# Performance work log

Measured on AMD Instinct MI355X. Metric: run time of the kernel, lower is better.

Reference implementation:

```python
import jax, jax.numpy as jnp
import numpy as np

N_NODES = 50000
N_EDGES = 800000
IN_DIM = 128
HID = 64
OUT = 32
HEADS = 2
NEG_SLOPE = 0.2  # PyG GATConv default


def _gat_layer(x, edge_index, W, a_src, a_dst, b, concat):
    """PyG-style GATConv (add_self_loops=True, eval mode so dropout is a no-op).
    x: [N, F_in], W: [F_in, H*C], a_src/a_dst: [H, C], b: [H*C] or [C].
    """
    N = x.shape[0]
    H, C = a_src.shape
    loops = jnp.arange(N, dtype=edge_index.dtype)
    src = jnp.concatenate([edge_index[0], loops])  # [E+N]
    dst = jnp.concatenate([edge_index[1], loops])

    h = (x @ W).reshape(N, H, C)                   # [N, H, C]
    alpha_src = jnp.sum(h * a_src, axis=-1)        # [N, H]
    alpha_dst = jnp.sum(h * a_dst, axis=-1)        # [N, H]

    e = jax.nn.leaky_relu(alpha_src[src] + alpha_dst[dst], NEG_SLOPE)  # [E+N, H]
    # segment softmax over incoming edges per destination node
    e_max = jax.ops.segment_max(e, dst, num_segments=N)               # [N, H]
    e_exp = jnp.exp(e - e_max[dst])
    denom = jax.ops.segment_sum(e_exp, dst, num_segments=N)           # [N, H]
    alpha = e_exp / denom[dst]                                        # [E+N, H]

    msg = h[src] * alpha[..., None]                                   # [E+N, H, C]
    out = jax.ops.segment_sum(msg, dst, num_segments=N)               # [N, H, C]
    if concat:
        return out.reshape(N, H * C) + b
    return out.mean(axis=1) + b


def setup_inputs() -> dict:
    key = jax.random.key(0)
    ks = jax.random.split(key, 10)
    x = jax.random.normal(ks[0], (N_NODES, IN_DIM), dtype=jnp.float32)
    edge_index = jax.random.randint(ks[1], (2, N_EDGES), 0, N_NODES, dtype=jnp.int64)
    s1 = 1.0 / np.sqrt(IN_DIM)
    s2 = 1.0 / np.sqrt(HEADS * HID)
    return {
        "x": x,
        "edge_index": edge_index,
        "W1": jax.random.normal(ks[2], (IN_DIM, HEADS * HID), dtype=jnp.float32) * s1,
        "a_src1": jax.random.normal(ks[3], (HEADS, HID), dtype=jnp.float32) * s2,
        "a_dst1": jax.random.normal(ks[4], (HEADS, HID), dtype=jnp.float32) * s2,
        "b1": jnp.zeros((HEADS * HID,), dtype=jnp.float32),
        "W2": jax.random.normal(ks[5], (HEADS * HID, OUT), dtype=jnp.float32) * s2,
        "a_src2": jax.random.normal(ks[6], (1, OUT), dtype=jnp.float32) * (1.0 / np.sqrt(OUT)),
        "a_dst2": jax.random.normal(ks[7], (1, OUT), dtype=jnp.float32) * (1.0 / np.sqrt(OUT)),
        "b2": jnp.zeros((OUT,), dtype=jnp.float32),
    }


def reference(x, edge_index, W1, a_src1, a_dst1, b1, W2, a_src2, a_dst2, b2):
    h = _gat_layer(x, edge_index, W1, a_src1, a_dst1, b1, concat=True)   # [N, HEADS*HID]
    h = jax.nn.relu(h)  # dropout is identity in eval mode
    out = _gat_layer(h, edge_index, W2, a_src2, a_dst2, b2, concat=False)  # [N, OUT]
    return out
```

## Files before the change

### kernel.cpp

```cpp
#include <hip/hip_runtime.h>

#define NEG 0.2f

constexpr int NB  = 196;
constexpr int PB  = 4608;
constexpr int EPB = 4096;

using short8 = __attribute__((ext_vector_type(8))) short;
using f32x4  = __attribute__((ext_vector_type(4))) float;

__device__ __forceinline__ ushort f2bf(float f) {
  uint u = __float_as_uint(f);
  return (ushort)((u + 0x7fffu + ((u >> 16) & 1u)) >> 16);
}
__device__ __forceinline__ float bflo(uint u) { return __uint_as_float(u << 16); }
__device__ __forceinline__ float bfhi(uint u) { return __uint_as_float(u & 0xffff0000u); }

__global__ void zero_kernel(int* __restrict__ p, int n)
{
  const int i = threadIdx.x;
  if (i < n) p[i] = 0;
}

__global__ void wt_kernel(const float* __restrict__ W, ushort* __restrict__ wtg)
{
  const int idx = blockIdx.x * 256 + threadIdx.x;
  const int n = idx >> 7, k = idx & 127;
  wtg[idx] = f2bf(W[k * 128 + n]);
}

__global__ __launch_bounds__(256) void binA_kernel(const int* __restrict__ ei,
                                                   int* __restrict__ bcursor,
                                                   int2* __restrict__ tmp, int E)
{
  __shared__ int cnt[NB];
  __shared__ int base[NB];
  const int t = threadIdx.x;
  const int e0 = blockIdx.x * EPB;
  const int e1 = min(e0 + EPB, E);

  if (t < NB) cnt[t] = 0;
  __syncthreads();
  for (int i = e0 + t; i < e1; i += 256)
    atomicAdd(&cnt[ei[E + i] >> 8], 1);
  __syncthreads();
  if (t < NB) {
    const int c = cnt[t];
    if (c > 0) base[t] = atomicAdd(&bcursor[t], c);
    cnt[t] = 0;
  }
  __syncthreads();
  for (int i = e0 + t; i < e1; i += 256) {
    const int s = ei[i];
    const int d = ei[E + i];
    const int b = d >> 8;
    const int pos = base[b] + atomicAdd(&cnt[b], 1);
    tmp[(size_t)b * PB + pos] = make_int2(s, d);
  }
}

__global__ __launch_bounds__(256) void binB_kernel(const int2* __restrict__ tmp,
                                                   const int* __restrict__ bcursor,
                                                   int2* __restrict__ offs2,
                                                   int* __restrict__ ssrc, int N)
{
  __shared__ int cnt[256];
  __shared__ int cur[256];
  __shared__ int sc[256];
  const int b = blockIdx.x;
  const int t = threadIdx.x;
  const int d0 = b << 8;
  const int beg = b * PB;
  const int cE = bcursor[b];

  cnt[t] = 0;
  __syncthreads();
  for (int i = t; i < cE; i += 256)
    atomicAdd(&cnt[tmp[beg + i].y - d0], 1);
  __syncthreads();
  sc[t] = cnt[t];
  __syncthreads();
  for (int off = 1; off < 256; off <<= 1) {
    int v = (t >= off) ? sc[t - off] : 0;
    __syncthreads();
    sc[t] += v;
    __syncthreads();
  }
  const int ebase = sc[t] - cnt[t];
  cur[t] = ebase;
  const int dst = d0 + t;
  if (dst < N) offs2[dst] = make_int2(beg + ebase, beg + ebase + cnt[t]);
  __syncthreads();
  for (int i = t; i < cE; i += 256) {
    const int2 e = tmp[beg + i];
    const int pos = beg + atomicAdd(&cur[e.y - d0], 1);
    ssrc[pos] = e.x;
  }
}

constexpr int BM1 = 64;

__global__ __launch_bounds__(256, 2) void gemm1_kernel(
    const float* __restrict__ x, const ushort* __restrict__ wtg,
    const float* __restrict__ a_src, const float* __restrict__ a_dst,
    ushort* __restrict__ h, float* __restrict__ asrc, float* __restrict__ adst,
    int N)
{
  __shared__ ushort xs[64][136];
  __shared__ ushort wt[128][136];
  const int t = threadIdx.x;
  const int n0 = blockIdx.x * BM1;

#pragma unroll
  for (int i = 0; i < 8; ++i) {
    const int idx = t + i * 256;
    const int row = idx >> 5;
    const int q   = idx & 31;
    int rn = n0 + row; if (rn >= N) rn = N - 1;
    const float4 v = *(const float4*)(x + (size_t)rn * 128 + q * 4);
    ushort4 o;
    o.x = f2bf(v.x); o.y = f2bf(v.y); o.z = f2bf(v.z); o.w = f2bf(v.w);
    *(ushort4*)&xs[row][q * 4] = o;
  }
#pragma unroll
  for (int i = 0; i < 8; ++i) {
    const int idx = t + i * 256;
    const int nr = idx >> 4;
    const int qq = idx & 15;
    const uint4 v = *(const uint4*)(wtg + (size_t)nr * 128 + qq * 8);
    *(uint4*)&wt[nr][qq * 8] = v;
  }
  __syncthreads();

  const int w   = t >> 6;
  const int l   = t & 63;
  const int c   = l & 15;
  const int g   = l >> 4;
  const int wr0 = w * 16;

  f32x4 acc[8];
#pragma unroll
  for (int nt = 0; nt < 8; ++nt) acc[nt] = {0.f, 0.f, 0.f, 0.f};

#pragma unroll
  for (int kc = 0; kc < 4; ++kc) {
    const int kb = kc * 32 + g * 8;
    const short8 af = *(const short8*)&xs[wr0 + c][kb];
#pragma unroll
    for (int nt = 0; nt < 8; ++nt) {
      const short8 bf = *(const short8*)&wt[nt * 16 + c][kb];
      acc[nt] = __builtin_amdgcn_mfma_f32_16x16x32_bf16(af, bf, acc[nt], 0, 0, 0);
    }
  }

  float pvs[2][4] = {{0.f,0.f,0.f,0.f},{0.f,0.f,0.f,0.f}};
  float pvd[2][4] = {{0.f,0.f,0.f,0.f},{0.f,0.f,0.f,0.f}};
#pragma unroll
  for (int nt = 0; nt < 8; ++nt) {
    const int col = nt * 16 + c;
    const float as = a_src[col];
    const float ad = a_dst[col];
    const int hd = nt >> 2;
#pragma unroll
    for (int r = 0; r < 4; ++r) {
      pvs[hd][r] += acc[nt][r] * as;
      pvd[hd][r] += acc[nt][r] * ad;
    }
  }
#pragma unroll
  for (int nt = 0; nt < 8; ++nt) {
    const int col = nt * 16 + c;
#pragma unroll
    for (int r = 0; r < 4; ++r) {
      const int nn = n0 + wr0 + g * 4 + r;
      if (nn < N) h[(size_t)nn * 128 + col] = f2bf(acc[nt][r]);
    }
  }
#pragma unroll
  for (int hd = 0; hd < 2; ++hd) {
#pragma unroll
    for (int r = 0; r < 4; ++r) {
#pragma unroll
      for (int m = 1; m <= 8; m <<= 1) {
        pvs[hd][r] += __shfl_xor(pvs[hd][r], m, 64);
        pvd[hd][r] += __shfl_xor(pvd[hd][r], m, 64);
      }
    }
  }
  if (c == 0) {
#pragma unroll
    for (int r = 0; r < 4; ++r) {
      const int nn = n0 + wr0 + g * 4 + r;
      if (nn < N) {
        asrc[nn * 2 + 0] = pvs[0][r];
        asrc[nn * 2 + 1] = pvs[1][r];
        adst[nn * 2 + 0] = pvd[0][r];
        adst[nn * 2 + 1] = pvd[1][r];
      }
    }
  }
}

constexpr int BM2 = 32;

__global__ __launch_bounds__(256, 4) void gemm2_kernel(
    const ushort* __restrict__ xb, const float* __restrict__ W,
    const float* __restrict__ a_src, const float* __restrict__ a_dst,
    float* __restrict__ h, float* __restrict__ asrc, float* __restrict__ adst,
    int N)
{
  __shared__ float xs[BM2][132];
  __shared__ float wsm[128][32];
  const int t = threadIdx.x;
  const int n0 = blockIdx.x * BM2;

#pragma unroll
  for (int i = 0; i < 2; ++i) {
    const int idx = t + i * 256;
    const int row = idx >> 4;
    const int sc  = idx & 15;
    int rn = n0 + row; if (rn >= N) rn = N - 1;
    const uint4 v = *(const uint4*)(xb + (size_t)rn * 128 + sc * 8);
    float* dp = &xs[row][sc * 8];
    dp[0] = bflo(v.x); dp[1] = bfhi(v.x);
    dp[2] = bflo(v.y); dp[3] = bfhi(v.y);
    dp[4] = bflo(v.z); dp[5] = bfhi(v.z);
    dp[6] = bflo(v.w); dp[7] = bfhi(v.w);
  }
#pragma unroll
  for (int i = 0; i < 4; ++i) {
    const int idx = t + i * 256;
    const int row = idx >> 3;
    const int cq  = idx & 7;
    *(float4*)&wsm[row][cq * 4] = *(const float4*)(W + row * 32 + cq * 4);
  }
  __syncthreads();

  const int c4 = (t & 7) << 2;
  const int tn = t >> 3;

  float4 acc = make_float4(0.f, 0.f, 0.f, 0.f);

#pragma unroll 4
  for (int k0 = 0; k0 < 128; k0 += 4) {
    const float4 w0 = *(const float4*)&wsm[k0 + 0][c4];
    const float4 w1 = *(const float4*)&wsm[k0 + 1][c4];
    const float4 w2 = *(const float4*)&wsm[k0 + 2][c4];
    const float4 w3 = *(const float4*)&wsm[k0 + 3][c4];
    const float4 xv = *(const float4*)&xs[tn][k0];
    acc.x += xv.x * w0.x + xv.y * w1.x + xv.z * w2.x + xv.w * w3.x;
    acc.y += xv.x * w0.y + xv.y * w1.y + xv.z * w2.y + xv.w * w3.y;
    acc.z += xv.x * w0.z + xv.y * w1.z + xv.z * w2.z + xv.w * w3.z;
    acc.w += xv.x * w0.w + xv.y * w1.w + xv.z * w2.w + xv.w * w3.w;
  }

  const int nn = n0 + tn;
  if (nn < N) {
    *(float4*)(h + (size_t)nn * 32 + c4) = acc;

    const float4 avs = *(const float4*)(a_src + c4);
    const float4 avd = *(const float4*)(a_dst + c4);
    float vs = acc.x * avs.x + acc.y * avs.y + acc.z * avs.z + acc.w * avs.w;
    float vd = acc.x * avd.x + acc.y * avd.y + acc.z * avd.z + acc.w * avd.w;
#pragma unroll
    for (int m = 1; m <= 4; m <<= 1) {
      vs += __shfl_xor(vs, m, 64);
      vd += __shfl_xor(vd, m, 64);
    }
    if ((t & 7) == 0) {
      asrc[nn] = vs;
      adst[nn] = vd;
    }
  }
}

__global__ __launch_bounds__(256) void agg1_kernel(
    const int2* __restrict__ offs2, const int* __restrict__ ssrc,
    const ushort* __restrict__ h, const float* __restrict__ asrc,
    const float* __restrict__ adst, const float* __restrict__ b,
    ushort* __restrict__ out, int N)
{
  const int n = (blockIdx.x * 256 + threadIdx.x) >> 6;
  const int lane = threadIdx.x & 63;
  const int sub = lane & 15;
  const int g = lane >> 4;
  const int head = sub >> 3;
  if (n >= N) return;

  const float2 adv = *(const float2*)(adst + 2 * n);
  const float advh = head ? adv.y : adv.x;

  float a0 = 0.f, a1 = 0.f, a2 = 0.f, a3 = 0.f;
  float a4 = 0.f, a5 = 0.f, a6 = 0.f, a7 = 0.f;
  float den = 0.f;

  const int2 be = offs2[n];
  const int beg = be.x, end = be.y;

  for (int i0 = beg + g; i0 < end; i0 += 16) {
    int    si[4];
    bool   vv[4];
    float2 av[4];
    uint4  gi[4];
#pragma unroll
    for (int j = 0; j < 4; ++j) {
      const int i = i0 + 4 * j;
      vv[j] = i < end;
      si[j] = vv[j] ? ssrc[i] : ssrc[i0];
    }
#pragma unroll
    for (int j = 0; j < 4; ++j)
      av[j] = *(const float2*)(asrc + 2 * si[j]);
#pragma unroll
    for (int j = 0; j < 4; ++j)
      gi[j] = *(const uint4*)(h + (size_t)si[j] * 128 + sub * 8);
#pragma unroll
    for (int j = 0; j < 4; ++j) {
      float e = (head ? av[j].y : av[j].x) + advh;
      e = e > 0.f ? e : NEG * e;
      const float w = vv[j] ? __expf(e) : 0.f;
      const uint4 gv = gi[j];
      den += w;
      a0 += w * bflo(gv.x); a1 += w * bfhi(gv.x);
      a2 += w * bflo(gv.y); a3 += w * bfhi(gv.y);
      a4 += w * bflo(gv.z); a5 += w * bfhi(gv.z);
      a6 += w * bflo(gv.w); a7 += w * bfhi(gv.w);
    }
  }

  if (g == 0) {
    const float2 asv = *(const float2*)(asrc + 2 * n);
    float e = (head ? asv.y : asv.x) + advh;
    e = e > 0.f ? e : NEG * e;
    const float w = __expf(e);
    den += w;
    const uint4 gv = *(const uint4*)(h + (size_t)n * 128 + sub * 8);
    a0 += w * bflo(gv.x); a1 += w * bfhi(gv.x);
    a2 += w * bflo(gv.y); a3 += w * bfhi(gv.y);
    a4 += w * bflo(gv.z); a5 += w * bfhi(gv.z);
    a6 += w * bflo(gv.w); a7 += w * bfhi(gv.w);
  }

#pragma unroll
  for (int m = 16; m <= 32; m <<= 1) {
    a0 += __shfl_xor(a0, m, 64); a1 += __shfl_xor(a1, m, 64);
    a2 += __shfl_xor(a2, m, 64); a3 += __shfl_xor(a3, m, 64);
    a4 += __shfl_xor(a4, m, 64); a5 += __shfl_xor(a5, m, 64);
    a6 += __shfl_xor(a6, m, 64); a7 += __shfl_xor(a7, m, 64);
    den += __shfl_xor(den, m, 64);
  }

  if (g == 0) {
    const float4 b0 = *(const float4*)(b + sub * 8);
    const float4 b1 = *(const float4*)(b + sub * 8 + 4);
    const float inv = 1.f / den;
    float r0 = a0 * inv + b0.x, r1 = a1 * inv + b0.y;
    float r2 = a2 * inv + b0.z, r3 = a3 * inv + b0.w;
    float r4 = a4 * inv + b1.x, r5 = a5 * inv + b1.y;
    float r6 = a6 * inv + b1.z, r7 = a7 * inv + b1.w;
    r0 = r0 > 0.f ? r0 : 0.f; r1 = r1 > 0.f ? r1 : 0.f;
    r2 = r2 > 0.f ? r2 : 0.f; r3 = r3 > 0.f ? r3 : 0.f;
    r4 = r4 > 0.f ? r4 : 0.f; r5 = r5 > 0.f ? r5 : 0.f;
    r6 = r6 > 0.f ? r6 : 0.f; r7 = r7 > 0.f ? r7 : 0.f;
    uint4 o;
    o.x = ((uint)f2bf(r1) << 16) | f2bf(r0);
    o.y = ((uint)f2bf(r3) << 16) | f2bf(r2);
    o.z = ((uint)f2bf(r5) << 16) | f2bf(r4);
    o.w = ((uint)f2bf(r7) << 16) | f2bf(r6);
    *(uint4*)(out + (size_t)n * 128 + sub * 8) = o;
  }
}

__global__ __launch_bounds__(256) void agg2_kernel(
    const int2* __restrict__ offs2, const int* __restrict__ ssrc,
    const float* __restrict__ h, const float* __restrict__ asrc,
    const float* __restrict__ adst, const float* __restrict__ b,
    float* __restrict__ out, int N)
{
  const int n = (blockIdx.x * 256 + threadIdx.x) >> 6;
  const int lane = threadIdx.x & 63;
  const int g = lane >> 3;
  const int c4 = (lane & 7) << 2;
  if (n >= N) return;

  const float adv = adst[n];
  float4 a = make_float4(0.f, 0.f, 0.f, 0.f);
  float den = 0.f;

  const int2 be = offs2[n];
  const int beg = be.x, end = be.y;

  for (int i0 = beg + g; i0 < end; i0 += 32) {
    int    si[4];
    bool   vv[4];
    float  av[4];
    float4 hi[4];
#pragma unroll
    for (int j = 0; j < 4; ++j) {
      const int i = i0 + 8 * j;
      vv[j] = i < end;
      si[j] = vv[j] ? ssrc[i] : ssrc[i0];
    }
#pragma unroll
    for (int j = 0; j < 4; ++j)
      av[j] = asrc[si[j]];
#pragma unroll
    for (int j = 0; j < 4; ++j)
      hi[j] = *(const float4*)(h + (size_t)si[j] * 32 + c4);
#pragma unroll
    for (int j = 0; j < 4; ++j) {
      float e = av[j] + adv;
      e = e > 0.f ? e : NEG * e;
      const float w = vv[j] ? __expf(e) : 0.f;
      den += w;
      a.x += w * hi[j].x;
      a.y += w * hi[j].y;
      a.z += w * hi[j].z;
      a.w += w * hi[j].w;
    }
  }

  if (g == 0) {
    float e = asrc[n] + adv;
    e = e > 0.f ? e : NEG * e;
    const float w = __expf(e);
    den += w;
    const float4 hv = *(const float4*)(h + (size_t)n * 32 + c4);
    a.x += w * hv.x; a.y += w * hv.y; a.z += w * hv.z; a.w += w * hv.w;
  }

#pragma unroll
  for (int m = 8; m <= 32; m <<= 1) {
    a.x += __shfl_xor(a.x, m, 64);
    a.y += __shfl_xor(a.y, m, 64);
    a.z += __shfl_xor(a.z, m, 64);
    a.w += __shfl_xor(a.w, m, 64);
    den += __shfl_xor(den, m, 64);
  }

  if (g == 0) {
    const float4 bv = *(const float4*)(b + c4);
    const float inv = 1.f / den;
    float4 r;
    r.x = a.x * inv + bv.x;
    r.y = a.y * inv + bv.y;
    r.z = a.z * inv + bv.z;
    r.w = a.w * inv + bv.w;
    *(float4*)(out + (size_t)n * 32 + c4) = r;
  }
}

extern "C" void kernel_launch(void* const* d_in, const int* in_sizes, int n_in,
                              void* d_out, int out_size, void* d_ws, size_t ws_size,
                              hipStream_t stream)
{
  const float* x   = (const float*)d_in[0];
  const int*   ei  = (const int*)  d_in[1];
  const float* W1  = (const float*)d_in[2];
  const float* as1 = (const float*)d_in[3];
  const float* ad1 = (const float*)d_in[4];
  const float* b1  = (const float*)d_in[5];
  const float* W2  = (const float*)d_in[6];
  const float* as2 = (const float*)d_in[7];
  const float* ad2 = (const float*)d_in[8];
  const float* b2  = (const float*)d_in[9];

  const int N = in_sizes[0] / 128;
  const int E = in_sizes[1] / 2;
  const size_t PT = (size_t)NB * PB;

  char* p = (char*)d_ws;
  int* bcursor  = (int*)p;               p += (size_t)NB * 4;
  int2* offs2   = (int2*)p;              p += (size_t)N * 8;
  int2* tmp     = (int2*)p;              p += PT * 8;
  int* ssrc     = (int*)p;               p += PT * 4;
  ushort* wtg   = (ushort*)p;            p += (size_t)128 * 128 * 2;
  ushort* h1    = (ushort*)p;            p += (size_t)N * 128 * 2;
  ushort* out1  = (ushort*)p;            p += (size_t)N * 128 * 2;
  float* asrc1  = (float*)p;             p += (size_t)N * 2 * 4;
  float* adst1  = (float*)p;             p += (size_t)N * 2 * 4;
  float* h2     = (float*)p;             p += (size_t)N * 32 * 4;
  float* asrc2  = (float*)p;             p += (size_t)N * 4;
  float* adst2  = (float*)p;             p += (size_t)N * 4;
  float* out    = (float*)d_out;

  const int nchunk = (E + EPB - 1) / EPB;

  zero_kernel<<<1, 256, 0, stream>>>(bcursor, NB);
  wt_kernel<<<64, 256, 0, stream>>>(W1, wtg);
  binA_kernel<<<nchunk, 256, 0, stream>>>(ei, bcursor, tmp, E);
  binB_kernel<<<NB, 256, 0, stream>>>(tmp, bcursor, offs2, ssrc, N);

  gemm1_kernel<<<(N + BM1 - 1) / BM1, 256, 0, stream>>>(x, wtg, as1, ad1,
                                                        h1, asrc1, adst1, N);
  agg1_kernel<<<(N * 64 + 255) / 256, 256, 0, stream>>>(offs2, ssrc, h1,
                                                        asrc1, adst1, b1, out1, N);

  gemm2_kernel<<<(N + BM2 - 1) / BM2, 256, 0, stream>>>(out1, W2, as2, ad2,
                                                        h2, asrc2, adst2, N);
  agg2_kernel<<<(N * 64 + 255) / 256, 256, 0, stream>>>(offs2, ssrc, h2,
                                                        asrc2, adst2, b2, out, N);
}
```

Baseline: 131.4 us.

## Use bf16 MFMA for layer-2 GEMM and store h2 as bf16

Rewrites the second-layer GEMM to use bf16 MFMA 16x16x32 instructions on a pre-transposed bf16 W2, in place of scalar fp32 FMAs. The layer-2 features h2 are now stored as bf16, which halves the bytes gathered per edge in agg2. The zero and W1-transpose kernels are merged into one prep kernel that also converts W2, saving a launch. The cost is lower precision in the layer-2 features and attention logits.

```diff
diff --git a/kernel.cpp b/kernel.cpp
--- a/kernel.cpp
+++ b/kernel.cpp
@@ -16,17 +16,22 @@
 __device__ __forceinline__ float bflo(uint u) { return __uint_as_float(u << 16); }
 __device__ __forceinline__ float bfhi(uint u) { return __uint_as_float(u & 0xffff0000u); }
 
-__global__ void zero_kernel(int* __restrict__ p, int n)
-{
-  const int i = threadIdx.x;
-  if (i < n) p[i] = 0;
-}
-
-__global__ void wt_kernel(const float* __restrict__ W, ushort* __restrict__ wtg)
-{
-  const int idx = blockIdx.x * 256 + threadIdx.x;
-  const int n = idx >> 7, k = idx & 127;
-  wtg[idx] = f2bf(W[k * 128 + n]);
+__global__ void prep_kernel(const float* __restrict__ W1, ushort* __restrict__ w1t,
+                            const float* __restrict__ W2, ushort* __restrict__ w2t,
+                            int* __restrict__ bcursor)
+{
+  const int b = blockIdx.x, t = threadIdx.x;
+  if (b < 64) {
+    const int idx = b * 256 + t;
+    const int n = idx >> 7, k = idx & 127;
+    w1t[idx] = f2bf(W1[k * 128 + n]);
+  } else {
+    for (int i = t; i < 4096; i += 256) {
+      const int n = i >> 7, k = i & 127;
+      w2t[i] = f2bf(W2[k * 32 + n]);
+    }
+    if (t < NB) bcursor[t] = 0;
+  }
 }
 
 __global__ __launch_bounds__(256) void binA_kernel(const int* __restrict__ ei,
@@ -201,75 +206,97 @@
   }
 }
 
-constexpr int BM2 = 32;
-
-__global__ __launch_bounds__(256, 4) void gemm2_kernel(
-    const ushort* __restrict__ xb, const float* __restrict__ W,
+constexpr int BM2 = 64;
+
+__global__ __launch_bounds__(256, 2) void gemm2_kernel(
+    const ushort* __restrict__ xb, const ushort* __restrict__ w2t,
     const float* __restrict__ a_src, const float* __restrict__ a_dst,
-    float* __restrict__ h, float* __restrict__ asrc, float* __restrict__ adst,
+    ushort* __restrict__ h, float* __restrict__ asrc, float* __restrict__ adst,
     int N)
 {
-  __shared__ float xs[BM2][132];
-  __shared__ float wsm[128][32];
+  __shared__ ushort xs[64][136];
+  __shared__ ushort wt[32][136];
   const int t = threadIdx.x;
   const int n0 = blockIdx.x * BM2;
 
 #pragma unroll
+  for (int i = 0; i < 4; ++i) {
+    const int idx = t + i * 256;
+    const int row = idx >> 4;
+    const int qq  = idx & 15;
+    int rn = n0 + row; if (rn >= N) rn = N - 1;
+    const uint4 v = *(const uint4*)(xb + (size_t)rn * 128 + qq * 8);
+    *(uint4*)&xs[row][qq * 8] = v;
+  }
+#pragma unroll
   for (int i = 0; i < 2; ++i) {
     const int idx = t + i * 256;
-    const int row = idx >> 4;
-    const int sc  = idx & 15;
-    int rn = n0 + row; if (rn >= N) rn = N - 1;
-    const uint4 v = *(const uint4*)(xb + (size_t)rn * 128 + sc * 8);
-    float* dp = &xs[row][sc * 8];
-    dp[0] = bflo(v.x); dp[1] = bfhi(v.x);
-    dp[2] = bflo(v.y); dp[3] = bfhi(v.y);
-    dp[4] = bflo(v.z); dp[5] = bfhi(v.z);
-    dp[6] = bflo(v.w); dp[7] = bfhi(v.w);
-  }
-#pragma unroll
-  for (int i = 0; i < 4; ++i) {
-    const int idx = t + i * 256;
-    const int row = idx >> 3;
-    const int cq  = idx & 7;
-    *(float4*)&wsm[row][cq * 4] = *(const float4*)(W + row * 32 + cq * 4);
-  }
-  __syncthreads();
-
-  const int c4 = (t & 7) << 2;
-  const int tn = t >> 3;
-
-  float4 acc = make_float4(0.f, 0.f, 0.f, 0.f);
-
-#pragma unroll 4
-  for (int k0 = 0; k0 < 128; k0 += 4) {
-    const float4 w0 = *(const float4*)&wsm[k0 + 0][c4];
-    const float4 w1 = *(const float4*)&wsm[k0 + 1][c4];
-    const float4 w2 = *(const float4*)&wsm[k0 + 2][c4];
-    const float4 w3 = *(const float4*)&wsm[k0 + 3][c4];
-    const float4 xv = *(const float4*)&xs[tn][k0];
-    acc.x += xv.x * w0.x + xv.y * w1.x + xv.z * w2.x + xv.w * w3.x;
-    acc.y += xv.x * w0.y + xv.y * w1.y + xv.z * w2.y + xv.w * w3.y;
-    acc.z += xv.x * w0.z + xv.y * w1.z + xv.z * w2.z + xv.w * w3.z;
-    acc.w += xv.x * w0.w + xv.y * w1.w + xv.z * w2.w + xv.w * w3.w;
-  }
-
-  const int nn = n0 + tn;
-  if (nn < N) {
-    *(float4*)(h + (size_t)nn * 32 + c4) = acc;
-
-    const float4 avs = *(const float4*)(a_src + c4);
-    const float4 avd = *(const float4*)(a_dst + c4);
-    float vs = acc.x * avs.x + acc.y * avs.y + acc.z * avs.z + acc.w * avs.w;
-    float vd = acc.x * avd.x + acc.y * avd.y + acc.z * avd.z + acc.w * avd.w;
-#pragma unroll
-    for (int m = 1; m <= 4; m <<= 1) {
-      vs += __shfl_xor(vs, m, 64);
-      vd += __shfl_xor(vd, m, 64);
-    }
-    if ((t & 7) == 0) {
-      asrc[nn] = vs;
-      adst[nn] = vd;
+    const int nr = idx >> 4;
+    const int qq = idx & 15;
+    const uint4 v = *(const uint4*)(w2t + (size_t)nr * 128 + qq * 8);
+    *(uint4*)&wt[nr][qq * 8] = v;
+  }
+  __syncthreads();
+
+  const int w   = t >> 6;
+  const int l   = t & 63;
+  const int c   = l & 15;
+  const int g   = l >> 4;
+  const int wr0 = w * 16;
+
+  f32x4 acc[2];
+  acc[0] = {0.f, 0.f, 0.f, 0.f};
+  acc[1] = {0.f, 0.f, 0.f, 0.f};
+
+#pragma unroll
+  for (int kc = 0; kc < 4; ++kc) {
+    const int kb = kc * 32 + g * 8;
+    const short8 af = *(const short8*)&xs[wr0 + c][kb];
+#pragma unroll
+    for (int nt = 0; nt < 2; ++nt) {
+      const short8 bf = *(const short8*)&wt[nt * 16 + c][kb];
+      acc[nt] = __builtin_amdgcn_mfma_f32_16x16x32_bf16(af, bf, acc[nt], 0, 0, 0);
+    }
+  }
+
+  float pvs[4] = {0.f, 0.f, 0.f, 0.f};
+  float pvd[4] = {0.f, 0.f, 0.f, 0.f};
+#pragma unroll
+  for (int nt = 0; nt < 2; ++nt) {
+    const int col = nt * 16 + c;
+    const float as = a_src[col];
+    const float ad = a_dst[col];
+#pragma unroll
+    for (int r = 0; r < 4; ++r) {
+      pvs[r] += acc[nt][r] * as;
+      pvd[r] += acc[nt][r] * ad;
+    }
+  }
+#pragma unroll
+  for (int nt = 0; nt < 2; ++nt) {
+    const int col = nt * 16 + c;
+#pragma unroll
+    for (int r = 0; r < 4; ++r) {
+      const int nn = n0 + wr0 + g * 4 + r;
+      if (nn < N) h[(size_t)nn * 32 + col] = f2bf(acc[nt][r]);
+    }
+  }
+#pragma unroll
+  for (int r = 0; r < 4; ++r) {
+#pragma unroll
+    for (int m = 1; m <= 8; m <<= 1) {
+      pvs[r] += __shfl_xor(pvs[r], m, 64);
+      pvd[r] += __shfl_xor(pvd[r], m, 64);
+    }
+  }
+  if (c == 0) {
+#pragma unroll
+    for (int r = 0; r < 4; ++r) {
+      const int nn = n0 + wr0 + g * 4 + r;
+      if (nn < N) {
+        asrc[nn] = pvs[r];
+        adst[nn] = pvd[r];
+      }
     }
   }
 }
@@ -373,7 +400,7 @@
 
 __global__ __launch_bounds__(256) void agg2_kernel(
     const int2* __restrict__ offs2, const int* __restrict__ ssrc,
-    const float* __restrict__ h, const float* __restrict__ asrc,
+    const ushort* __restrict__ h, const float* __restrict__ asrc,
     const float* __restrict__ adst, const float* __restrict__ b,
     float* __restrict__ out, int N)
 {
@@ -391,10 +418,10 @@
   const int beg = be.x, end = be.y;
 
   for (int i0 = beg + g; i0 < end; i0 += 32) {
-    int    si[4];
-    bool   vv[4];
-    float  av[4];
-    float4 hi[4];
+    int   si[4];
+    bool  vv[4];
+    float av[4];
+    uint2 ui[4];
 #pragma unroll
     for (int j = 0; j < 4; ++j) {
       const int i = i0 + 8 * j;
@@ -406,17 +433,17 @@
       av[j] = asrc[si[j]];
 #pragma unroll
     for (int j = 0; j < 4; ++j)
-      hi[j] = *(const float4*)(h + (size_t)si[j] * 32 + c4);
+      ui[j] = *(const uint2*)(h + (size_t)si[j] * 32 + c4);
 #pragma unroll
     for (int j = 0; j < 4; ++j) {
       float e = av[j] + adv;
       e = e > 0.f ? e : NEG * e;
       const float w = vv[j] ? __expf(e) : 0.f;
       den += w;
-      a.x += w * hi[j].x;
-      a.y += w * hi[j].y;
-      a.z += w * hi[j].z;
-      a.w += w * hi[j].w;
+      a.x += w * bflo(ui[j].x);
+      a.y += w * bfhi(ui[j].x);
+      a.z += w * bflo(ui[j].y);
+      a.w += w * bfhi(ui[j].y);
     }
   }
 
@@ -425,8 +452,9 @@
     e = e > 0.f ? e : NEG * e;
     const float w = __expf(e);
     den += w;
-    const float4 hv = *(const float4*)(h + (size_t)n * 32 + c4);
-    a.x += w * hv.x; a.y += w * hv.y; a.z += w * hv.z; a.w += w * hv.w;
+    const uint2 hv = *(const uint2*)(h + (size_t)n * 32 + c4);
+    a.x += w * bflo(hv.x); a.y += w * bfhi(hv.x);
+    a.z += w * bflo(hv.y); a.w += w * bfhi(hv.y);
   }
 
 #pragma unroll
@@ -474,29 +502,29 @@
   int2* offs2   = (int2*)p;              p += (size_t)N * 8;
   int2* tmp     = (int2*)p;              p += PT * 8;
   int* ssrc     = (int*)p;               p += PT * 4;
-  ushort* wtg   = (ushort*)p;            p += (size_t)128 * 128 * 2;
+  ushort* w1t   = (ushort*)p;            p += (size_t)128 * 128 * 2;
+  ushort* w2t   = (ushort*)p;            p += (size_t)32 * 128 * 2;
   ushort* h1    = (ushort*)p;            p += (size_t)N * 128 * 2;
   ushort* out1  = (ushort*)p;            p += (size_t)N * 128 * 2;
+  ushort* h2    = (ushort*)p;            p += (size_t)N * 32 * 2;
   float* asrc1  = (float*)p;             p += (size_t)N * 2 * 4;
   float* adst1  = (float*)p;             p += (size_t)N * 2 * 4;
-  float* h2     = (float*)p;             p += (size_t)N * 32 * 4;
   float* asrc2  = (float*)p;             p += (size_t)N * 4;
   float* adst2  = (float*)p;             p += (size_t)N * 4;
   float* out    = (float*)d_out;
 
   const int nchunk = (E + EPB - 1) / EPB;
 
-  zero_kernel<<<1, 256, 0, stream>>>(bcursor, NB);
-  wt_kernel<<<64, 256, 0, stream>>>(W1, wtg);
+  prep_kernel<<<65, 256, 0, stream>>>(W1, w1t, W2, w2t, bcursor);
   binA_kernel<<<nchunk, 256, 0, stream>>>(ei, bcursor, tmp, E);
   binB_kernel<<<NB, 256, 0, stream>>>(tmp, bcursor, offs2, ssrc, N);
 
-  gemm1_kernel<<<(N + BM1 - 1) / BM1, 256, 0, stream>>>(x, wtg, as1, ad1,
+  gemm1_kernel<<<(N + BM1 - 1) / BM1, 256, 0, stream>>>(x, w1t, as1, ad1,
                                                         h1, asrc1, adst1, N);
   agg1_kernel<<<(N * 64 + 255) / 256, 256, 0, stream>>>(offs2, ssrc, h1,
                                                         asrc1, adst1, b1, out1, N);
 
-  gemm2_kernel<<<(N + BM2 - 1) / BM2, 256, 0, stream>>>(out1, W2, as2, ad2,
+  gemm2_kernel<<<(N + BM2 - 1) / BM2, 256, 0, stream>>>(out1, w2t, as2, ad2,
                                                         h2, asrc2, adst2, N);
   agg2_kernel<<<(N * 64 + 255) / 256, 256, 0, stream>>>(offs2, ssrc, h2,
                                                         asrc2, adst2, b2, out, N);
```

Result: faster. 119.3 us (-9.2%).
